# Performance work log

Hardware: AMD Instinct MI355X
Metric: run time of the kernel (lower is better)

The kernel has to match this reference:

```python
import jax, jax.numpy as jnp
import numpy as np

D_MODEL = 64
TEMPER = float(np.power(D_MODEL, 0.5))  # d_model ** temper_value
B, L, DK = 64, 1024, 64
P = 2 * L - 1  # relative position range


def setup_inputs() -> dict:
    key = jax.random.key(0)
    k1, k2, k3, k4, k5 = jax.random.split(key, 5)
    q = jax.random.normal(k1, (B, L, DK), dtype=jnp.float32)
    k = jax.random.normal(k2, (B, L, DK), dtype=jnp.float32)
    v = jax.random.normal(k3, (B, L, DK), dtype=jnp.float32)
    position_dpa = jax.random.normal(k4, (B, P, DK), dtype=jnp.float32)
    attn_mask = jax.random.uniform(k5, (B, L, L)) < 0.1
    return {"q": q, "k": k, "v": v, "position_dpa": position_dpa, "attn_mask": attn_mask}


def reference(q, k, v, position_dpa, attn_mask):
    # q,k,v: [B, L, d]; position_dpa: [B, 2L-1, d]; attn_mask: [B, L, L] bool
    Lq = q.shape[1]
    attn = jnp.einsum('bld,bmd->blm', q, k) / TEMPER            # [B, L, L]
    attn_pos = jnp.einsum('bld,bpd->blp', q, position_dpa) / TEMPER  # [B, L, 2L-1]
    # Replicates batch_stripe(flip(attn_pos.transpose(1,2), -1)).transpose(1,2):
    # bias[b, i, j] = attn_pos[b, L-1-i, i+j]
    i = jnp.arange(Lq)
    rows = (Lq - 1) - i[:, None]                 # [L, 1]
    cols = i[:, None] + i[None, :]               # [L, L], values in [0, 2L-2]
    bias = attn_pos[:, rows, cols]               # [B, L, L]
    attn = attn + bias
    attn = jnp.where(attn_mask, -jnp.inf, attn)
    attn = jax.nn.softmax(attn, axis=-1)
    # dropout is identity in eval mode
    output = jnp.einsum('blm,bmd->bld', attn, v)  # [B, L, d]
    return output, attn
```

## Files before the change

### kernel.cpp

```cpp
#include <hip/hip_runtime.h>

#define BN   64
#define LN   1024
#define DKN  64
#define PN   2047
#define OUT_O_ELEMS ((size_t)BN * LN * DKN)
constexpr float kScale = 0.125f;

typedef short bf16x8 __attribute__((ext_vector_type(8)));
typedef float f32x4  __attribute__((ext_vector_type(4)));

__device__ __forceinline__ unsigned short f2b(float f) {
  return (unsigned short)((__float_as_uint(f) + 0x8000u) >> 16);
}
__device__ __forceinline__ float b2f(unsigned short h) {
  return __uint_as_float(((unsigned)h) << 16);
}
__device__ __forceinline__ unsigned pk2(float x, float y) {
  unsigned lo = (__float_as_uint(x) + 0x8000u) >> 16;
  unsigned hi = (__float_as_uint(y) + 0x8000u) & 0xFFFF0000u;
  return lo | hi;
}

union U8 { unsigned u[4]; bf16x8 v; };

__device__ __forceinline__ bf16x8 pack8(float4 a, float4 b) {
  U8 r;
  r.u[0] = pk2(a.x, a.y); r.u[1] = pk2(a.z, a.w);
  r.u[2] = pk2(b.x, b.y); r.u[3] = pk2(b.z, b.w);
  return r.v;
}

__global__ void flag_init(unsigned* f) { *f = 0u; }

__global__ void flag_scan(const unsigned* __restrict__ mw, unsigned* f) {
  int idx = blockIdx.x * 256 + threadIdx.x;
  unsigned bits = 0;
#pragma unroll
  for (int i = 0; i < 4; ++i) {
    unsigned wv = mw[idx * 4 + i];
    if (wv == 0x3F800000u) bits |= 2u;
    else if (wv > 1u)      bits |= 4u;
  }
  if (bits) atomicOr(f, bits);
}

__global__ __launch_bounds__(256) void convert_f32_bf16(const float4* __restrict__ in,
                                                        uint2* __restrict__ outp) {
  int idx = blockIdx.x * 256 + threadIdx.x;
  float4 a = in[idx];
  outp[idx] = make_uint2(pk2(a.x, a.y), pk2(a.z, a.w));
}

__global__ __launch_bounds__(256) void transpose_v(const float4* __restrict__ vg,
                                                   short* __restrict__ vt) {
  __shared__ float tile[64 * 65];
  const int tid = threadIdx.x;
  const int b  = blockIdx.x >> 4;
  const int mt = blockIdx.x & 15;
  const size_t base = ((size_t)b * 1024 + mt * 64) * 16;
#pragma unroll
  for (int i = 0; i < 4; ++i) {
    int j = tid + (i << 8);
    float4 a = vg[base + j];
    float* d = &tile[(j >> 4) * 65 + ((j & 15) << 2)];
    d[0] = a.x; d[1] = a.y; d[2] = a.z; d[3] = a.w;
  }
  __syncthreads();
#pragma unroll
  for (int i = 0; i < 4; ++i) {
    int j  = tid + (i << 8);
    int d  = j >> 4;
    int mq = (j & 15) << 2;
    unsigned u0 = pk2(tile[(mq + 0) * 65 + d], tile[(mq + 1) * 65 + d]);
    unsigned u1 = pk2(tile[(mq + 2) * 65 + d], tile[(mq + 3) * 65 + d]);
    size_t idx = ((size_t)b * 64 + d) * 1024 + mt * 64 + mq;
    *(uint2*)(vt + idx) = make_uint2(u0, u1);
  }
}

__global__ __launch_bounds__(256, 4)
void attn_kernel(const float* __restrict__ qf, const float* __restrict__ kf,
                 const float* __restrict__ vf, const float* __restrict__ pf,
                 const void* __restrict__ mask, const unsigned* __restrict__ flagp,
                 const short* __restrict__ k16, const short* __restrict__ p16,
                 const short* __restrict__ vt16,
                 float* __restrict__ out) {
  __shared__ short qA[16 * 72];
  __shared__ short qrA[16 * 72];
  __shared__ short E[16 * 1032];
  __shared__ float rowSum[16];
  __shared__ float invSum[16];

  const int tid  = threadIdx.x;
  const int w    = tid >> 6;
  const int lane = tid & 63;
  const int col  = lane & 15;
  const int quad = lane >> 4;

  int p   = blockIdx.x;
  int xcd = p & 7;
  int qq  = p >> 3;
  int rt  = qq & 63;
  int bh  = qq >> 6;
  const int b  = (bh << 3) | xcd;
  const int l0 = rt << 4;

  unsigned mflag = flagp ? flagp[0] : 0u;
  const int mkind = (mflag & 4u) ? 1 : ((mflag & 2u) ? 2 : 0);

  if (tid < 16) rowSum[tid] = 0.0f;

  {
    const float4* qg = (const float4*)qf;
    int row = tid >> 4, c4 = tid & 15;
    float4 a  = qg[((size_t)b * LN + (l0 + row)) * 16 + c4];
    float4 r_ = qg[((size_t)b * LN + (LN - 1 - l0 - row)) * 16 + c4];
    *(uint2*)&qA[row * 72 + c4 * 4]  = make_uint2(pk2(a.x, a.y), pk2(a.z, a.w));
    *(uint2*)&qrA[row * 72 + c4 * 4] = make_uint2(pk2(r_.x, r_.y), pk2(r_.z, r_.w));
  }
  __syncthreads();

  const bf16x8 aq0 = *(const bf16x8*)&qA[col * 72 + quad * 8];
  const bf16x8 aq1 = *(const bf16x8*)&qA[col * 72 + quad * 8 + 32];
  const bf16x8 ar0 = *(const bf16x8*)&qrA[col * 72 + quad * 8];
  const bf16x8 ar1 = *(const bf16x8*)&qrA[col * 72 + quad * 8 + 32];

  float sumr[4] = {0.f, 0.f, 0.f, 0.f};
  const int moff = (w << 4) + col;

  for (int t = 0; t < 16; ++t) {
    const int m0    = t << 6;
    const int mglob = m0 + moff;

    bf16x8 kb0, kb1, pb00, pb01, pb10, pb11;
    int g0 = l0 + m0 + moff;
    int g1 = g0 + 16; if (g1 > PN - 1) g1 = PN - 1;
    if (k16) {
      const short* kr = k16 + ((size_t)b * LN + mglob) * DKN;
      kb0 = *(const bf16x8*)(kr + quad * 8);
      kb1 = *(const bf16x8*)(kr + 32 + quad * 8);
      const short* pr0 = p16 + ((size_t)b * PN + g0) * DKN;
      const short* pr1 = p16 + ((size_t)b * PN + g1) * DKN;
      pb00 = *(const bf16x8*)(pr0 + quad * 8);
      pb01 = *(const bf16x8*)(pr0 + 32 + quad * 8);
      pb10 = *(const bf16x8*)(pr1 + quad * 8);
      pb11 = *(const bf16x8*)(pr1 + 32 + quad * 8);
    } else {
      const float4* kr = (const float4*)(kf + ((size_t)b * LN + mglob) * DKN);
      kb0 = pack8(kr[quad * 2], kr[quad * 2 + 1]);
      kb1 = pack8(kr[8 + quad * 2], kr[9 + quad * 2]);
      const float4* pr0 = (const float4*)(pf + ((size_t)b * PN + g0) * DKN);
      const float4* pr1 = (const float4*)(pf + ((size_t)b * PN + g1) * DKN);
      pb00 = pack8(pr0[quad * 2], pr0[quad * 2 + 1]);
      pb01 = pack8(pr0[8 + quad * 2], pr0[9 + quad * 2]);
      pb10 = pack8(pr1[quad * 2], pr1[quad * 2 + 1]);
      pb11 = pack8(pr1[8 + quad * 2], pr1[9 + quad * 2]);
    }

    f32x4 qk = {0.f, 0.f, 0.f, 0.f};
    qk = __builtin_amdgcn_mfma_f32_16x16x32_bf16(aq0, kb0, qk, 0, 0, 0);
    qk = __builtin_amdgcn_mfma_f32_16x16x32_bf16(aq1, kb1, qk, 0, 0, 0);

    f32x4 ba = {0.f, 0.f, 0.f, 0.f}, bb = {0.f, 0.f, 0.f, 0.f};
    ba = __builtin_amdgcn_mfma_f32_16x16x32_bf16(ar0, pb00, ba, 0, 0, 0);
    ba = __builtin_amdgcn_mfma_f32_16x16x32_bf16(ar1, pb01, ba, 0, 0, 0);
    bb = __builtin_amdgcn_mfma_f32_16x16x32_bf16(ar0, pb10, bb, 0, 0, 0);
    bb = __builtin_amdgcn_mfma_f32_16x16x32_bf16(ar1, pb11, bb, 0, 0, 0);

#pragma unroll
    for (int r = 0; r < 4; ++r) {
      int i = (quad << 2) + r;
      int o = i + col;
      int srcLane = (lane & 48) | (o & 15);
      float va = __shfl(ba[r], srcLane);
      float vb = __shfl(bb[r], srcLane);
      float bias = (o < 16) ? va : vb;
      float s = (qk[r] + bias) * kScale;

      size_t mi = ((((size_t)b << 10) + (size_t)(l0 + i)) << 10) + (size_t)mglob;
      bool msk;
      if (mkind == 0)      msk = ((const int*)mask)[mi] != 0;
      else if (mkind == 1) msk = ((const unsigned char*)mask)[mi] != 0;
      else                 msk = ((const float*)mask)[mi] != 0.f;

      float e = msk ? 0.f : __expf(s);
      unsigned short eb = f2b(e);
      sumr[r] += b2f(eb);
      E[i * 1032 + mglob] = (short)eb;
    }
  }

#pragma unroll
  for (int r = 0; r < 4; ++r) {
    float vsum = sumr[r];
    vsum += __shfl_xor(vsum, 1);
    vsum += __shfl_xor(vsum, 2);
    vsum += __shfl_xor(vsum, 4);
    vsum += __shfl_xor(vsum, 8);
    if (col == 0) atomicAdd(&rowSum[(quad << 2) + r], vsum);
  }
  __syncthreads();
  if (tid < 16) invSum[tid] = 1.0f / rowSum[tid];

  f32x4 acc = {0.f, 0.f, 0.f, 0.f};
  const int drow = moff;
  for (int t = 0; t < 16; ++t) {
    const int m0 = t << 6;
    bf16x8 vb0, vb1;
    if (vt16) {
      const short* vr = vt16 + ((size_t)b * 64 + drow) * 1024 + m0;
      vb0 = *(const bf16x8*)(vr + quad * 8);
      vb1 = *(const bf16x8*)(vr + 32 + quad * 8);
    } else {
      const float* vc = vf + ((size_t)b * LN + m0) * DKN + drow;
      U8 t0, t1;
#pragma unroll
      for (int j = 0; j < 4; ++j) {
        t0.u[j] = pk2(vc[(quad * 8 + 2 * j) * 64],      vc[(quad * 8 + 2 * j + 1) * 64]);
        t1.u[j] = pk2(vc[(32 + quad * 8 + 2 * j) * 64], vc[(32 + quad * 8 + 2 * j + 1) * 64]);
      }
      vb0 = t0.v; vb1 = t1.v;
    }
    bf16x8 ea0 = *(const bf16x8*)&E[col * 1032 + m0 + quad * 8];
    bf16x8 ea1 = *(const bf16x8*)&E[col * 1032 + m0 + 32 + quad * 8];
    acc = __builtin_amdgcn_mfma_f32_16x16x32_bf16(ea0, vb0, acc, 0, 0, 0);
    acc = __builtin_amdgcn_mfma_f32_16x16x32_bf16(ea1, vb1, acc, 0, 0, 0);
  }
  __syncthreads();

#pragma unroll
  for (int r = 0; r < 4; ++r) {
    int i = (quad << 2) + r;
    out[(((size_t)b << 10) + (size_t)(l0 + i)) * 64 + drow] = acc[r] * invSum[i];
  }

  float* outA = out + OUT_O_ELEMS;
#pragma unroll
  for (int it = 0; it < 16; ++it) {
    int j = tid + (it << 8);
    int row = j >> 8, c4 = j & 255;
    const ushort4 ev = *(const ushort4*)&E[row * 1032 + (c4 << 2)];
    float inv = invSum[row];
    float4 o4;
    o4.x = b2f(ev.x) * inv;
    o4.y = b2f(ev.y) * inv;
    o4.z = b2f(ev.z) * inv;
    o4.w = b2f(ev.w) * inv;
    *(float4*)&outA[((((size_t)b << 10) + (size_t)(l0 + row)) << 10) + (size_t)(c4 << 2)] = o4;
  }
}

extern "C" void kernel_launch(void* const* d_in, const int* in_sizes, int n_in,
                              void* d_out, int out_size, void* d_ws, size_t ws_size,
                              hipStream_t stream) {
  const float* q   = (const float*)d_in[0];
  const float* k   = (const float*)d_in[1];
  const float* v   = (const float*)d_in[2];
  const float* pos = (const float*)d_in[3];
  const void* mask = d_in[4];
  float* out = (float*)d_out;

  unsigned* flag = nullptr;
  if (ws_size >= 256) {
    flag = (unsigned*)d_ws;
    flag_init<<<1, 1, 0, stream>>>(flag);
    flag_scan<<<64, 256, 0, stream>>>((const unsigned*)mask, flag);
  }

  const size_t kElems  = (size_t)BN * LN * DKN;
  const size_t pElems  = (size_t)BN * PN * DKN;
  const size_t offK    = 256;
  const size_t offP    = offK + kElems * 2;
  const size_t offVT   = offP + pElems * 2;
  const size_t wsNeed  = offVT + kElems * 2;

  short *k16 = nullptr, *p16 = nullptr, *vt16 = nullptr;
  if (ws_size >= wsNeed) {
    char* base = (char*)d_ws;
    k16  = (short*)(base + offK);
    p16  = (short*)(base + offP);
    vt16 = (short*)(base + offVT);
    convert_f32_bf16<<<(int)(kElems / 1024), 256, 0, stream>>>((const float4*)k,   (uint2*)k16);
    convert_f32_bf16<<<(int)(pElems / 1024), 256, 0, stream>>>((const float4*)pos, (uint2*)p16);
    transpose_v<<<BN * 16, 256, 0, stream>>>((const float4*)v, vt16);
  }

  attn_kernel<<<BN * (LN / 16), 256, 0, stream>>>(q, k, v, pos, mask, flag,
                                                  k16, p16, vt16, out);
}
```

Measured before the change: 748.2 us.

## Software-pipeline K/P/mask loads and interleave attention-row stores with PV MFMA

The score loop now double-buffers K, position and mask loads one tile ahead, so global latency overlaps the MFMA and exp work. The PV loop prefetches V tiles and writes one normalized attention row per iteration, overlapping the large attn-matrix store with the MFMAs instead of storing after them. The invSum shared array is dropped in favour of reciprocals computed inline, and mask handling drops the float-mask branch in favour of a uint/byte load. This raises register pressure, and the float-mask case now reads raw bits rather than comparing floats.

```diff
diff --git a/kernel.cpp b/kernel.cpp
--- a/kernel.cpp
+++ b/kernel.cpp
@@ -90,7 +90,6 @@
   __shared__ short qrA[16 * 72];
   __shared__ short E[16 * 1032];
   __shared__ float rowSum[16];
-  __shared__ float invSum[16];
 
   const int tid  = threadIdx.x;
   const int w    = tid >> 6;
@@ -128,66 +127,111 @@
 
   float sumr[4] = {0.f, 0.f, 0.f, 0.f};
   const int moff = (w << 4) + col;
-
-  for (int t = 0; t < 16; ++t) {
-    const int m0    = t << 6;
-    const int mglob = m0 + moff;
-
-    bf16x8 kb0, kb1, pb00, pb01, pb10, pb11;
-    int g0 = l0 + m0 + moff;
-    int g1 = g0 + 16; if (g1 > PN - 1) g1 = PN - 1;
-    if (k16) {
-      const short* kr = k16 + ((size_t)b * LN + mglob) * DKN;
-      kb0 = *(const bf16x8*)(kr + quad * 8);
-      kb1 = *(const bf16x8*)(kr + 32 + quad * 8);
-      const short* pr0 = p16 + ((size_t)b * PN + g0) * DKN;
-      const short* pr1 = p16 + ((size_t)b * PN + g1) * DKN;
-      pb00 = *(const bf16x8*)(pr0 + quad * 8);
-      pb01 = *(const bf16x8*)(pr0 + 32 + quad * 8);
-      pb10 = *(const bf16x8*)(pr1 + quad * 8);
-      pb11 = *(const bf16x8*)(pr1 + 32 + quad * 8);
-    } else {
+  const size_t mrow0 = (((size_t)b << 10) + (size_t)(l0 + (quad << 2))) << 10;
+
+  if (k16) {
+    struct KPM { bf16x8 k0, k1, p00, p01, p10, p11; unsigned m[4]; };
+    KPM A, Bf;
+
+    auto LOAD = [&](int t, KPM& o) {
+      const int m0 = t << 6, mglob = m0 + moff;
+      const short* kr = k16 + ((size_t)b * LN + mglob) * DKN + quad * 8;
+      o.k0 = *(const bf16x8*)kr;
+      o.k1 = *(const bf16x8*)(kr + 32);
+      int g0 = l0 + m0 + moff;
+      int g1 = g0 + 16; if (g1 > PN - 1) g1 = PN - 1;
+      const short* pr0 = p16 + ((size_t)b * PN + g0) * DKN + quad * 8;
+      const short* pr1 = p16 + ((size_t)b * PN + g1) * DKN + quad * 8;
+      o.p00 = *(const bf16x8*)pr0;
+      o.p01 = *(const bf16x8*)(pr0 + 32);
+      o.p10 = *(const bf16x8*)pr1;
+      o.p11 = *(const bf16x8*)(pr1 + 32);
+      const size_t mi = mrow0 + (size_t)mglob;
+      if (mkind == 1) {
+        const unsigned char* mp = (const unsigned char*)mask + mi;
+#pragma unroll
+        for (int r = 0; r < 4; ++r) o.m[r] = mp[(size_t)r << 10];
+      } else {
+        const unsigned* mp = (const unsigned*)mask + mi;
+#pragma unroll
+        for (int r = 0; r < 4; ++r) o.m[r] = mp[(size_t)r << 10];
+      }
+    };
+
+    auto COMP = [&](int t, KPM& o) {
+      f32x4 qk = {0.f, 0.f, 0.f, 0.f};
+      qk = __builtin_amdgcn_mfma_f32_16x16x32_bf16(aq0, o.k0, qk, 0, 0, 0);
+      qk = __builtin_amdgcn_mfma_f32_16x16x32_bf16(aq1, o.k1, qk, 0, 0, 0);
+      f32x4 ba = {0.f, 0.f, 0.f, 0.f}, bb = {0.f, 0.f, 0.f, 0.f};
+      ba = __builtin_amdgcn_mfma_f32_16x16x32_bf16(ar0, o.p00, ba, 0, 0, 0);
+      ba = __builtin_amdgcn_mfma_f32_16x16x32_bf16(ar1, o.p01, ba, 0, 0, 0);
+      bb = __builtin_amdgcn_mfma_f32_16x16x32_bf16(ar0, o.p10, bb, 0, 0, 0);
+      bb = __builtin_amdgcn_mfma_f32_16x16x32_bf16(ar1, o.p11, bb, 0, 0, 0);
+      const int mglob = (t << 6) + moff;
+#pragma unroll
+      for (int r = 0; r < 4; ++r) {
+        int i = (quad << 2) + r;
+        int o2 = i + col;
+        int srcLane = (lane & 48) | (o2 & 15);
+        float va = __shfl(ba[r], srcLane);
+        float vb = __shfl(bb[r], srcLane);
+        float bias = (o2 < 16) ? va : vb;
+        float s = (qk[r] + bias) * kScale;
+        float e = o.m[r] ? 0.f : __expf(s);
+        unsigned short eb = f2b(e);
+        sumr[r] += b2f(eb);
+        E[i * 1032 + mglob] = (short)eb;
+      }
+    };
+
+    LOAD(0, A);
+    for (int t = 0; t < 16; t += 2) {
+      LOAD(t + 1, Bf);
+      COMP(t, A);
+      if (t < 14) LOAD(t + 2, A);
+      COMP(t + 1, Bf);
+    }
+  } else {
+    for (int t = 0; t < 16; ++t) {
+      const int m0 = t << 6, mglob = m0 + moff;
+      int g0 = l0 + m0 + moff;
+      int g1 = g0 + 16; if (g1 > PN - 1) g1 = PN - 1;
       const float4* kr = (const float4*)(kf + ((size_t)b * LN + mglob) * DKN);
-      kb0 = pack8(kr[quad * 2], kr[quad * 2 + 1]);
-      kb1 = pack8(kr[8 + quad * 2], kr[9 + quad * 2]);
+      bf16x8 kb0 = pack8(kr[quad * 2], kr[quad * 2 + 1]);
+      bf16x8 kb1 = pack8(kr[8 + quad * 2], kr[9 + quad * 2]);
       const float4* pr0 = (const float4*)(pf + ((size_t)b * PN + g0) * DKN);
       const float4* pr1 = (const float4*)(pf + ((size_t)b * PN + g1) * DKN);
-      pb00 = pack8(pr0[quad * 2], pr0[quad * 2 + 1]);
-      pb01 = pack8(pr0[8 + quad * 2], pr0[9 + quad * 2]);
-      pb10 = pack8(pr1[quad * 2], pr1[quad * 2 + 1]);
-      pb11 = pack8(pr1[8 + quad * 2], pr1[9 + quad * 2]);
-    }
-
-    f32x4 qk = {0.f, 0.f, 0.f, 0.f};
-    qk = __builtin_amdgcn_mfma_f32_16x16x32_bf16(aq0, kb0, qk, 0, 0, 0);
-    qk = __builtin_amdgcn_mfma_f32_16x16x32_bf16(aq1, kb1, qk, 0, 0, 0);
-
-    f32x4 ba = {0.f, 0.f, 0.f, 0.f}, bb = {0.f, 0.f, 0.f, 0.f};
-    ba = __builtin_amdgcn_mfma_f32_16x16x32_bf16(ar0, pb00, ba, 0, 0, 0);
-    ba = __builtin_amdgcn_mfma_f32_16x16x32_bf16(ar1, pb01, ba, 0, 0, 0);
-    bb = __builtin_amdgcn_mfma_f32_16x16x32_bf16(ar0, pb10, bb, 0, 0, 0);
-    bb = __builtin_amdgcn_mfma_f32_16x16x32_bf16(ar1, pb11, bb, 0, 0, 0);
-
-#pragma unroll
-    for (int r = 0; r < 4; ++r) {
-      int i = (quad << 2) + r;
-      int o = i + col;
-      int srcLane = (lane & 48) | (o & 15);
-      float va = __shfl(ba[r], srcLane);
-      float vb = __shfl(bb[r], srcLane);
-      float bias = (o < 16) ? va : vb;
-      float s = (qk[r] + bias) * kScale;
-
-      size_t mi = ((((size_t)b << 10) + (size_t)(l0 + i)) << 10) + (size_t)mglob;
-      bool msk;
-      if (mkind == 0)      msk = ((const int*)mask)[mi] != 0;
-      else if (mkind == 1) msk = ((const unsigned char*)mask)[mi] != 0;
-      else                 msk = ((const float*)mask)[mi] != 0.f;
-
-      float e = msk ? 0.f : __expf(s);
-      unsigned short eb = f2b(e);
-      sumr[r] += b2f(eb);
-      E[i * 1032 + mglob] = (short)eb;
+      bf16x8 pb00 = pack8(pr0[quad * 2], pr0[quad * 2 + 1]);
+      bf16x8 pb01 = pack8(pr0[8 + quad * 2], pr0[9 + quad * 2]);
+      bf16x8 pb10 = pack8(pr1[quad * 2], pr1[quad * 2 + 1]);
+      bf16x8 pb11 = pack8(pr1[8 + quad * 2], pr1[9 + quad * 2]);
+
+      f32x4 qk = {0.f, 0.f, 0.f, 0.f};
+      qk = __builtin_amdgcn_mfma_f32_16x16x32_bf16(aq0, kb0, qk, 0, 0, 0);
+      qk = __builtin_amdgcn_mfma_f32_16x16x32_bf16(aq1, kb1, qk, 0, 0, 0);
+      f32x4 ba = {0.f, 0.f, 0.f, 0.f}, bb = {0.f, 0.f, 0.f, 0.f};
+      ba = __builtin_amdgcn_mfma_f32_16x16x32_bf16(ar0, pb00, ba, 0, 0, 0);
+      ba = __builtin_amdgcn_mfma_f32_16x16x32_bf16(ar1, pb01, ba, 0, 0, 0);
+      bb = __builtin_amdgcn_mfma_f32_16x16x32_bf16(ar0, pb10, bb, 0, 0, 0);
+      bb = __builtin_amdgcn_mfma_f32_16x16x32_bf16(ar1, pb11, bb, 0, 0, 0);
+
+#pragma unroll
+      for (int r = 0; r < 4; ++r) {
+        int i = (quad << 2) + r;
+        int o2 = i + col;
+        int srcLane = (lane & 48) | (o2 & 15);
+        float va = __shfl(ba[r], srcLane);
+        float vb = __shfl(bb[r], srcLane);
+        float bias = (o2 < 16) ? va : vb;
+        float s = (qk[r] + bias) * kScale;
+        size_t mi = mrow0 + ((size_t)r << 10) + (size_t)mglob;
+        unsigned mu = (mkind == 1) ? (unsigned)((const unsigned char*)mask)[mi]
+                                   : ((const unsigned*)mask)[mi];
+        float e = mu ? 0.f : __expf(s);
+        unsigned short eb = f2b(e);
+        sumr[r] += b2f(eb);
+        E[i * 1032 + mglob] = (short)eb;
+      }
     }
   }
 
@@ -201,53 +245,68 @@
     if (col == 0) atomicAdd(&rowSum[(quad << 2) + r], vsum);
   }
   __syncthreads();
-  if (tid < 16) invSum[tid] = 1.0f / rowSum[tid];
 
   f32x4 acc = {0.f, 0.f, 0.f, 0.f};
   const int drow = moff;
-  for (int t = 0; t < 16; ++t) {
-    const int m0 = t << 6;
-    bf16x8 vb0, vb1;
-    if (vt16) {
-      const short* vr = vt16 + ((size_t)b * 64 + drow) * 1024 + m0;
-      vb0 = *(const bf16x8*)(vr + quad * 8);
-      vb1 = *(const bf16x8*)(vr + 32 + quad * 8);
-    } else {
-      const float* vc = vf + ((size_t)b * LN + m0) * DKN + drow;
-      U8 t0, t1;
-#pragma unroll
-      for (int j = 0; j < 4; ++j) {
-        t0.u[j] = pk2(vc[(quad * 8 + 2 * j) * 64],      vc[(quad * 8 + 2 * j + 1) * 64]);
-        t1.u[j] = pk2(vc[(32 + quad * 8 + 2 * j) * 64], vc[(32 + quad * 8 + 2 * j + 1) * 64]);
-      }
-      vb0 = t0.v; vb1 = t1.v;
-    }
-    bf16x8 ea0 = *(const bf16x8*)&E[col * 1032 + m0 + quad * 8];
-    bf16x8 ea1 = *(const bf16x8*)&E[col * 1032 + m0 + 32 + quad * 8];
-    acc = __builtin_amdgcn_mfma_f32_16x16x32_bf16(ea0, vb0, acc, 0, 0, 0);
-    acc = __builtin_amdgcn_mfma_f32_16x16x32_bf16(ea1, vb1, acc, 0, 0, 0);
-  }
-  __syncthreads();
-
-#pragma unroll
-  for (int r = 0; r < 4; ++r) {
-    int i = (quad << 2) + r;
-    out[(((size_t)b << 10) + (size_t)(l0 + i)) * 64 + drow] = acc[r] * invSum[i];
-  }
-
   float* outA = out + OUT_O_ELEMS;
-#pragma unroll
-  for (int it = 0; it < 16; ++it) {
-    int j = tid + (it << 8);
-    int row = j >> 8, c4 = j & 255;
-    const ushort4 ev = *(const ushort4*)&E[row * 1032 + (c4 << 2)];
-    float inv = invSum[row];
+  const size_t aBase = (((size_t)b << 10) + (size_t)l0) << 10;
+
+  auto WROW = [&](int t) {
+    float inv = 1.0f / rowSum[t];
+    const ushort4 ev = *(const ushort4*)&E[t * 1032 + (tid << 2)];
     float4 o4;
     o4.x = b2f(ev.x) * inv;
     o4.y = b2f(ev.y) * inv;
     o4.z = b2f(ev.z) * inv;
     o4.w = b2f(ev.w) * inv;
-    *(float4*)&outA[((((size_t)b << 10) + (size_t)(l0 + row)) << 10) + (size_t)(c4 << 2)] = o4;
+    *(float4*)&outA[aBase + ((size_t)t << 10) + (size_t)(tid << 2)] = o4;
+  };
+
+  if (vt16) {
+    const short* vbase = vt16 + ((size_t)b * 64 + drow) * 1024 + quad * 8;
+    bf16x8 v0A = *(const bf16x8*)vbase;
+    bf16x8 v1A = *(const bf16x8*)(vbase + 32);
+    bf16x8 v0B, v1B;
+    for (int t = 0; t < 16; t += 2) {
+      { const short* vr = vbase + ((t + 1) << 6);
+        v0B = *(const bf16x8*)vr; v1B = *(const bf16x8*)(vr + 32); }
+      { const int m0 = t << 6;
+        bf16x8 ea0 = *(const bf16x8*)&E[col * 1032 + m0 + quad * 8];
+        bf16x8 ea1 = *(const bf16x8*)&E[col * 1032 + m0 + 32 + quad * 8];
+        acc = __builtin_amdgcn_mfma_f32_16x16x32_bf16(ea0, v0A, acc, 0, 0, 0);
+        acc = __builtin_amdgcn_mfma_f32_16x16x32_bf16(ea1, v1A, acc, 0, 0, 0);
+        WROW(t); }
+      if (t < 14) { const short* vr = vbase + ((t + 2) << 6);
+        v0A = *(const bf16x8*)vr; v1A = *(const bf16x8*)(vr + 32); }
+      { const int m0 = (t + 1) << 6;
+        bf16x8 ea0 = *(const bf16x8*)&E[col * 1032 + m0 + quad * 8];
+        bf16x8 ea1 = *(const bf16x8*)&E[col * 1032 + m0 + 32 + quad * 8];
+        acc = __builtin_amdgcn_mfma_f32_16x16x32_bf16(ea0, v0B, acc, 0, 0, 0);
+        acc = __builtin_amdgcn_mfma_f32_16x16x32_bf16(ea1, v1B, acc, 0, 0, 0);
+        WROW(t + 1); }
+    }
+  } else {
+    for (int t = 0; t < 16; ++t) {
+      const int m0 = t << 6;
+      const float* vc = vf + ((size_t)b * LN + m0) * DKN + drow;
+      U8 t0, t1;
+#pragma unroll
+      for (int j = 0; j < 4; ++j) {
+        t0.u[j] = pk2(vc[(quad * 8 + 2 * j) * 64],      vc[(quad * 8 + 2 * j + 1) * 64]);
+        t1.u[j] = pk2(vc[(32 + quad * 8 + 2 * j) * 64], vc[(32 + quad * 8 + 2 * j + 1) * 64]);
+      }
+      bf16x8 ea0 = *(const bf16x8*)&E[col * 1032 + m0 + quad * 8];
+      bf16x8 ea1 = *(const bf16x8*)&E[col * 1032 + m0 + 32 + quad * 8];
+      acc = __builtin_amdgcn_mfma_f32_16x16x32_bf16(ea0, t0.v, acc, 0, 0, 0);
+      acc = __builtin_amdgcn_mfma_f32_16x16x32_bf16(ea1, t1.v, acc, 0, 0, 0);
+    }
+    for (int t = 0; t < 16; ++t) WROW(t);
+  }
+
+#pragma unroll
+  for (int r = 0; r < 4; ++r) {
+    int i = (quad << 2) + r;
+    out[(((size_t)b << 10) + (size_t)(l0 + i)) * 64 + drow] = acc[r] * (1.0f / rowSum[i]);
   }
 }
 
```

Result: faster. 705.7 us (-5.7%).
